# Optimization experiments

Measured on AMD Instinct MI355X. Metric: run time of the kernel, lower is better.

The kernel has to match this reference:

```python
import jax, jax.numpy as jnp
import numpy as np

S_LEN = 256   # seq_len
B = 512       # batch
STATE = 32    # state_dim
ZD = 64       # z_dim
RNN = 512     # rnn_dim
HD = 512      # h_dim
LOG2PI = float(np.log(2.0 * np.pi))


def setup_inputs() -> dict:
    key = jax.random.key(0)
    ks = jax.random.split(key, 12)

    def mat(k, shape, fan_in):
        return jax.random.normal(k, shape, dtype=jnp.float32) * (1.0 / np.sqrt(fan_in))

    z32 = lambda *s: jnp.zeros(s, jnp.float32)
    return {
        "states": jax.random.normal(ks[0], (S_LEN, B, STATE), jnp.float32),
        "z": jax.random.normal(ks[1], (B, ZD), jnp.float32),
        # GRU layer 0: input = concat(state, action) -> 2*STATE
        "Wih0": mat(ks[2], (3 * RNN, 2 * STATE), 2 * STATE),
        "Whh0": mat(ks[3], (3 * RNN, RNN), RNN),
        "bih0": z32(3 * RNN),
        "bhh0": z32(3 * RNN),
        # GRU layer 1: input = hidden of layer 0
        "Wih1": mat(ks[4], (3 * RNN, RNN), RNN),
        "Whh1": mat(ks[5], (3 * RNN, RNN), RNN),
        "bih1": z32(3 * RNN),
        "bhh1": z32(3 * RNN),
        # dec_action_fc: Linear(STATE+ZD+RNN -> HD), ReLU, Linear(HD -> HD), ReLU
        "Wfc1": mat(ks[6], (HD, STATE + ZD + RNN), STATE + ZD + RNN),
        "bfc1": z32(HD),
        "Wfc2": mat(ks[7], (HD, HD), HD),
        "bfc2": z32(HD),
        "Wmean": mat(ks[8], (STATE, HD), HD),
        "bmean": z32(STATE),
        "Wlv": mat(ks[9], (STATE, HD), HD),
        "blv": z32(STATE),
    }


def _gru_step(x, h, Wih, Whh, bih, bhh):
    # PyTorch GRUCell math
    gi = x @ Wih.T + bih  # [B, 3R]
    gh = h @ Whh.T + bhh
    ir, iz, inn = jnp.split(gi, 3, axis=1)
    hr, hz, hn = jnp.split(gh, 3, axis=1)
    r = jax.nn.sigmoid(ir + hr)
    zg = jax.nn.sigmoid(iz + hz)
    n = jnp.tanh(inn + r * hn)
    return (1.0 - zg) * n + zg * h


def reference(states, z, Wih0, Whh0, bih0, bhh0, Wih1, Whh1, bih1, bhh1,
              Wfc1, bfc1, Wfc2, bfc2, Wmean, bmean, Wlv, blv):
    # actions[t] = states[t+1] - states[t]
    actions = states[1:] - states[:-1]
    # loop runs for actions.size(0)-1 = T-2 steps using (states[t], actions[t])
    xs = (states[:-2], actions[:-1])
    Bb = z.shape[0]
    R = Whh0.shape[1]
    h_init = jnp.zeros((2, Bb, R), states.dtype)
    nll_init = jnp.zeros((Bb, states.shape[-1]), states.dtype)

    def step(carry, xt):
        h, nll = carry
        s, a = xt  # [B, STATE] each
        # decode_action: cat(state, z, hidden[-1]) -> MLP -> mean, logvar
        fc_in = jnp.concatenate([s, z, h[1]], axis=1)
        dh = jax.nn.relu(fc_in @ Wfc1.T + bfc1)
        dh = jax.nn.relu(dh @ Wfc2.T + bfc2)
        mean = dh @ Wmean.T + bmean
        logvar = dh @ Wlv.T + blv
        # nll -= Normal(mean, logvar).log_prob(action), std = exp(0.5*logvar)
        nll_t = 0.5 * ((a - mean) ** 2 * jnp.exp(-logvar) + logvar + LOG2PI)
        # update_hidden_state with cat(state, action) through 2-layer GRU
        x_in = jnp.concatenate([s, a], axis=1)
        h0n = _gru_step(x_in, h[0], Wih0, Whh0, bih0, bhh0)
        h1n = _gru_step(h0n, h[1], Wih1, Whh1, bih1, bhh1)
        return (jnp.stack([h0n, h1n]), nll + nll_t), None

    (h, nll), _ = jax.lax.scan(step, (h_init, nll_init), xs)
    return nll  # accumulated NLL, shape [B, STATE]
```

## Files before the change

### kernel.cpp

```cpp
#include <hip/hip_runtime.h>
#include <math.h>

#define BATCH 512
#define LOG2PI 1.8378770664093453f
#define HB 262144

typedef __attribute__((ext_vector_type(8))) short bfrag;
typedef __attribute__((ext_vector_type(4))) float f32x4;
typedef __attribute__((ext_vector_type(4))) unsigned int u32x4;

#define MFMA(a,b,c) __builtin_amdgcn_mfma_f32_16x16x32_bf16(a,b,c,0,0,0)
#define ASTORE(p,v) __hip_atomic_store((p),(v),__ATOMIC_RELAXED,__HIP_MEMORY_SCOPE_AGENT)
#define ALOAD(p)    __hip_atomic_load((p),__ATOMIC_RELAXED,__HIP_MEMORY_SCOPE_AGENT)

__device__ __forceinline__ void st16_sc1(void* p, u32x4 v){
  asm volatile("global_store_dwordx4 %0, %1, off sc1" :: "v"(p), "v"(v) : "memory");
}

__device__ __forceinline__ float sigm(float x){ return 1.0f/(1.0f+__expf(-x)); }
__device__ __forceinline__ unsigned short f2bf(float f){
  unsigned int u = __builtin_bit_cast(unsigned int, f);
  u += 0x7FFFu + ((u>>16)&1u);
  return (unsigned short)(u>>16);
}
__device__ __forceinline__ bfrag cvt8(const float* __restrict__ p){
  bfrag v;
  #pragma unroll
  for (int e=0;e<8;++e) v[e] = (short)f2bf(p[e]);
  return v;
}
__device__ __forceinline__ bfrag cvt8d(const float* __restrict__ p1, const float* __restrict__ p0){
  bfrag v;
  #pragma unroll
  for (int e=0;e<8;++e) v[e] = (short)f2bf(p1[e]-p0[e]);
  return v;
}

struct Params {
  const float *states, *zin;
  const float *Wih0, *Whh0, *bih0, *bhh0;
  const float *Wih1, *Whh1, *bih1, *bhh1;
  const float *Wfc1, *bfc1, *Wfc2, *bfc2;
  const float *Wmean, *bmean, *Wlv, *blv;
  unsigned short *act;
  float *out;
};

__global__ __launch_bounds__(256, 1) void fused(Params P, unsigned* flags) {
  __shared__ unsigned short sm[74752];
  const int tid  = threadIdx.x;
  const int lane = tid & 63;
  const int wv   = tid >> 6;
  const int r16  = lane & 15, kg = lane >> 4;
  const int blk  = blockIdx.x;
  const int xg   = blk & 7, sub = blk >> 3;

  unsigned short* h0 = P.act;
  unsigned short* h1 = P.act +  8*(size_t)HB;
  unsigned short* d1 = P.act + 16*(size_t)HB;
  unsigned short* d2 = P.act + 24*(size_t)HB;

  if (xg < 4) {
    const int jt = sub;
    const float* Wsrc[2] = {P.Wih1, P.Whh1};
    #pragma unroll
    for (int m = 0; m < 2; ++m) {
      const float* W = Wsrc[m];
      for (int c = tid; c < 3072; c += 256) {
        int g = c >> 10, rem = c & 1023;
        int r = rem >> 6, k = (rem & 63) << 3;
        *(bfrag*)&sm[(g*16+r)*1032 + m*512 + k] =
          cvt8(&W[((size_t)(g*512 + jt*16 + r))*512 + k]);
      }
    }
  } else if (xg < 6) {
    const int jt = sub;
    for (int c = tid; c < 384; c += 256) {
      int g = c >> 7, rem = c & 127;
      int r = rem >> 3, k = (rem & 7) << 3;
      *(bfrag*)&sm[(g*16+r)*584 + k] =
        cvt8(&P.Wih0[((size_t)(g*512 + jt*16 + r))*64 + k]);
    }
    for (int c = tid; c < 3072; c += 256) {
      int g = c >> 10, rem = c & 1023;
      int r = rem >> 6, k = (rem & 63) << 3;
      *(bfrag*)&sm[(g*16+r)*584 + 64 + k] =
        cvt8(&P.Whh0[((size_t)(g*512 + jt*16 + r))*512 + k]);
    }
  } else if (xg == 6) {
    const int bn = (sub & 7) * 64;
    const int bmB = (sub >> 3) * 128;
    for (int c = tid; c < 4864; c += 256) {
      int n = c / 76, k = (c % 76) << 3;
      *(bfrag*)&sm[n*616 + k] = cvt8(&P.Wfc1[(size_t)(bn + n)*608 + k]);
    }
    for (int c = tid; c < 1024; c += 256) {
      int r = c >> 3, k = (c & 7) << 3;
      *(bfrag*)&sm[47616 + r*64 + k] = cvt8(&P.zin[(size_t)(bmB + r)*64 + k]);
    }
  } else {
    const int bn = (sub & 7) * 64;
    for (int c = tid; c < 4096; c += 256) {
      int n = c >> 6, k = (c & 63) << 3;
      *(bfrag*)&sm[n*520 + k] = cvt8(&P.Wfc2[(size_t)(bn + n)*512 + k]);
    }
    for (int c = tid; c < 4096; c += 256) {
      int m = c >> 6, k = (c & 63) << 3;
      const float* src = (m < 32) ? &P.Wmean[(size_t)m*512 + k]
                                  : &P.Wlv[(size_t)(m-32)*512 + k];
      *(bfrag*)&sm[33280 + m*520 + k] = cvt8(src);
    }
  }

  float b0 = 0.f, b1 = 0.f, b2 = 0.f, b3 = 0.f;
  if (xg < 4) {
    int j = sub*16 + r16;
    b0 = P.bih1[j] + P.bhh1[j];
    b1 = P.bih1[j+512] + P.bhh1[j+512];
    b2 = P.bih1[j+1024]; b3 = P.bhh1[j+1024];
  } else if (xg < 6) {
    int j = sub*16 + r16;
    b0 = P.bih0[j] + P.bhh0[j];
    b1 = P.bih0[j+512] + P.bhh0[j+512];
    b2 = P.bih0[j+1024]; b3 = P.bhh0[j+1024];
  } else if (xg == 6) {
    int nn0 = (sub & 7)*64 + (wv&1)*32 + r16;
    b0 = P.bfc1[nn0]; b1 = P.bfc1[nn0+16];
  } else {
    int nn0 = (sub & 7)*64 + (wv&1)*32 + r16;
    b0 = P.bfc2[nn0]; b1 = P.bfc2[nn0+16];
    int c = wv*16 + r16;
    b2 = (c < 32) ? P.bmean[c] : P.blv[c-32];
  }
  float hs[4][4] = {};
  float nacc0 = 0.f, nacc1 = 0.f;

  for (int u = 0; u <= 256; ++u) {
    if (wv == 0) {
      int pb1 = -1, pb2 = -1;
      const unsigned t1 = (unsigned)u, t2 = (unsigned)(u - 6);
      if (xg >= 4 && xg < 6) {
        if (u >= 1 && lane < 32) pb1 = lane*8 + xg;
        if (u >= 7)              pb2 = (lane>>1)*8 + 2*(xg-4) + (lane&1);
      } else if (xg < 4) {
        if (u >= 1) pb1 = (lane < 32) ? lane*8 + xg : (lane-32)*8 + 4 + (xg>>1);
        if (u >= 7 && lane < 8) pb2 = (xg*8 + lane)*8 + 6;
      } else if (xg == 6) {
        if (u >= 1 && lane < 32) pb1 = lane*8 + (sub>>3);
        if (u >= 7 && lane < 8)  pb2 = ((sub & ~7) + lane)*8 + 7;
      } else {
        if (u >= 1 && lane < 16) pb1 = ((sub & ~7) + (lane&7))*8 + ((lane<8)?6:7);
      }
      unsigned spin = 0;
      while (true) {
        bool ok = true;
        if (pb1 >= 0) ok &= (ALOAD(&flags[pb1*16]) >= t1);
        if (pb2 >= 0) ok &= (ALOAD(&flags[pb2*16]) >= t2);
        if (__all(ok)) break;
        if (++spin > (1u<<26)) break;
        __builtin_amdgcn_s_sleep(1);
      }
    }
    __syncthreads();
    if (tid < 64) __builtin_amdgcn_fence(__ATOMIC_ACQUIRE, "agent");
    __syncthreads();

    const int ju  = u & 7;
    const int jm1 = (u+7) & 7;
    const int jm2 = (u+6) & 7;
    const int jm3 = (u+5) & 7;

    if (xg < 4) {
      if (u >= 1 && u <= 254) {
        const int jt = sub, bmB = xg * 128;
        const unsigned short* h0r = h0 + (size_t)jm1*HB;
        const unsigned short* h1r = h1 + (size_t)jm2*HB;
        f32x4 R[2]={}, Z[2]={}, NI[2]={}, NH[2]={};
        const int row0 = bmB + wv*32 + r16;
        #pragma unroll
        for (int half = 0; half < 2; ++half) {
          const unsigned short* asrc = half ? h1r : h0r;
          #pragma unroll 4
          for (int kt = 0; kt < 16; ++kt) {
            const int kk = kt*32 + kg*8;
            const int kl = half*512 + kk;
            bfrag a0 = *(const bfrag*)&asrc[(size_t)row0*512 + kk];
            bfrag a1 = *(const bfrag*)&asrc[(size_t)(row0+16)*512 + kk];
            bfrag bR = *(const bfrag*)&sm[(0*16+r16)*1032 + kl];
            bfrag bZ = *(const bfrag*)&sm[(1*16+r16)*1032 + kl];
            bfrag bN = *(const bfrag*)&sm[(2*16+r16)*1032 + kl];
            R[0]=MFMA(a0,bR,R[0]); R[1]=MFMA(a1,bR,R[1]);
            Z[0]=MFMA(a0,bZ,Z[0]); Z[1]=MFMA(a1,bZ,Z[1]);
            if (!half) { NI[0]=MFMA(a0,bN,NI[0]); NI[1]=MFMA(a1,bN,NI[1]); }
            else       { NH[0]=MFMA(a0,bN,NH[0]); NH[1]=MFMA(a1,bN,NH[1]); }
          }
        }
        unsigned short* exch = sm + 49536;
        #pragma unroll
        for (int fm = 0; fm < 2; ++fm)
          #pragma unroll
          for (int e = 0; e < 4; ++e) {
            int rl = wv*32 + fm*16 + kg*4 + e;
            float r  = sigm(R[fm][e] + b0);
            float zg = sigm(Z[fm][e] + b1);
            float nn = tanhf(NI[fm][e] + b2 + r*(NH[fm][e] + b3));
            float hn = (1.f - zg)*nn + zg*hs[fm][e];
            hs[fm][e] = hn;
            exch[rl*16 + r16] = f2bf(hn);
          }
        __syncthreads();
        {
          unsigned short* dst = h1 + (size_t)jm1*HB;
          int r = tid >> 1, hc = tid & 1;
          u32x4 v = *(const u32x4*)&exch[r*16 + hc*8];
          st16_sc1(dst + ((size_t)(bmB + r))*512 + jt*16 + hc*8, v);
        }
      }
    } else if (xg < 6) {
      if (u <= 253) {
        const int jt = sub, bmB = (xg - 4) * 256;
        const unsigned short* h0r = h0 + (size_t)jm1*HB;
        const float* s0p = P.states + (size_t)u*BATCH*32;
        f32x4 R[4]={}, Z[4]={}, NI[4]={}, NH[4]={};
        #pragma unroll
        for (int ks = 0; ks < 2; ++ks) {
          const int kl = ks*32 + kg*8;
          bfrag a[4];
          #pragma unroll
          for (int fm = 0; fm < 4; ++fm) {
            int row = bmB + wv*64 + fm*16 + r16;
            a[fm] = (ks == 0)
              ? cvt8(&s0p[(size_t)row*32 + kg*8])
              : cvt8d(&s0p[(size_t)(BATCH + row)*32 + kg*8], &s0p[(size_t)row*32 + kg*8]);
          }
          bfrag bR = *(const bfrag*)&sm[(0*16+r16)*584 + kl];
          bfrag bZ = *(const bfrag*)&sm[(1*16+r16)*584 + kl];
          bfrag bN = *(const bfrag*)&sm[(2*16+r16)*584 + kl];
          #pragma unroll
          for (int fm = 0; fm < 4; ++fm) {
            R[fm]=MFMA(a[fm],bR,R[fm]); Z[fm]=MFMA(a[fm],bZ,Z[fm]); NI[fm]=MFMA(a[fm],bN,NI[fm]);
          }
        }
        #pragma unroll 2
        for (int kt = 0; kt < 16; ++kt) {
          const int kk = kt*32 + kg*8;
          const int kl = 64 + kk;
          bfrag a[4];
          #pragma unroll
          for (int fm = 0; fm < 4; ++fm) {
            int row = bmB + wv*64 + fm*16 + r16;
            a[fm] = *(const bfrag*)&h0r[(size_t)row*512 + kk];
          }
          bfrag bR = *(const bfrag*)&sm[(0*16+r16)*584 + kl];
          bfrag bZ = *(const bfrag*)&sm[(1*16+r16)*584 + kl];
          bfrag bN = *(const bfrag*)&sm[(2*16+r16)*584 + kl];
          #pragma unroll
          for (int fm = 0; fm < 4; ++fm) {
            R[fm]=MFMA(a[fm],bR,R[fm]); Z[fm]=MFMA(a[fm],bZ,Z[fm]); NH[fm]=MFMA(a[fm],bN,NH[fm]);
          }
        }
        unsigned short* exch = sm + 28032;
        #pragma unroll
        for (int fm = 0; fm < 4; ++fm)
          #pragma unroll
          for (int e = 0; e < 4; ++e) {
            int rl = wv*64 + fm*16 + kg*4 + e;
            float r  = sigm(R[fm][e] + b0);
            float zg = sigm(Z[fm][e] + b1);
            float nn = tanhf(NI[fm][e] + b2 + r*(NH[fm][e] + b3));
            float hn = (1.f - zg)*nn + zg*hs[fm][e];
            hs[fm][e] = hn;
            exch[rl*16 + r16] = f2bf(hn);
          }
        __syncthreads();
        {
          unsigned short* dst = h0 + (size_t)ju*HB;
          int r = tid;
          u32x4 v0 = *(const u32x4*)&exch[r*16];
          u32x4 v1 = *(const u32x4*)&exch[r*16 + 8];
          unsigned short* dp = dst + ((size_t)(bmB + r))*512 + jt*16;
          st16_sc1(dp,     v0);
          st16_sc1(dp + 8, v1);
        }
      }
    } else if (xg == 6) {
      if (u >= 1 && u <= 254) {
        const int bmB = (sub >> 3) * 128, bnB = (sub & 7) * 64;
        const unsigned short* h1r = h1 + (size_t)jm2*HB;
        const float* s0p = P.states + (size_t)(u-1)*BATCH*32;
        f32x4 acc[4][2] = {};
        const int arow = bmB + (wv>>1)*64;
        const int bcol = (wv&1)*32;
        #pragma unroll 2
        for (int kt = 0; kt < 19; ++kt) {
          const int k = kt*32 + kg*8;
          bfrag a[4];
          #pragma unroll
          for (int fm = 0; fm < 4; ++fm) {
            int row = arow + fm*16 + r16;
            int rl  = row - bmB;
            if (kt == 0)      a[fm] = cvt8(&s0p[(size_t)row*32 + k]);
            else if (kt <= 2) a[fm] = *(const bfrag*)&sm[47616 + rl*64 + (k - 32)];
            else              a[fm] = *(const bfrag*)&h1r[(size_t)row*512 + (k - 96)];
          }
          bfrag bf0 = *(const bfrag*)&sm[(bcol      + r16)*616 + k];
          bfrag bf1 = *(const bfrag*)&sm[(bcol + 16 + r16)*616 + k];
          #pragma unroll
          for (int fm = 0; fm < 4; ++fm) {
            acc[fm][0] = MFMA(a[fm], bf0, acc[fm][0]);
            acc[fm][1] = MFMA(a[fm], bf1, acc[fm][1]);
          }
        }
        unsigned short* exch = sm + 39424;
        #pragma unroll
        for (int fm = 0; fm < 4; ++fm)
          #pragma unroll
          for (int fn = 0; fn < 2; ++fn) {
            float bias = fn ? b1 : b0;
            #pragma unroll
            for (int e = 0; e < 4; ++e) {
              int rl = (wv>>1)*64 + fm*16 + kg*4 + e;
              int cl = bcol + fn*16 + r16;
              exch[rl*64 + cl] = f2bf(fmaxf(acc[fm][fn][e] + bias, 0.f));
            }
          }
        __syncthreads();
        {
          unsigned short* dst = d1 + (size_t)jm1*HB;
          int r = tid >> 1, hc = tid & 1;
          #pragma unroll
          for (int q = 0; q < 4; ++q) {
            u32x4 v = *(const u32x4*)&exch[r*64 + hc*32 + q*8];
            st16_sc1(dst + ((size_t)(bmB + r))*512 + bnB + hc*32 + q*8, v);
          }
        }
        __syncthreads();
      }
    } else {
      if (u >= 2 && u <= 255) {
        const int bmB = (sub >> 3) * 128, bnB = (sub & 7) * 64;
        const unsigned short* dr = d1 + (size_t)jm2*HB;
        f32x4 acc[4][2] = {};
        const int arow = bmB + (wv>>1)*64;
        const int bcol = (wv&1)*32;
        #pragma unroll 2
        for (int kt = 0; kt < 16; ++kt) {
          const int k = kt*32 + kg*8;
          bfrag a[4];
          #pragma unroll
          for (int fm = 0; fm < 4; ++fm) {
            int row = arow + fm*16 + r16;
            a[fm] = *(const bfrag*)&dr[(size_t)row*512 + k];
          }
          bfrag bf0 = *(const bfrag*)&sm[(bcol      + r16)*520 + k];
          bfrag bf1 = *(const bfrag*)&sm[(bcol + 16 + r16)*520 + k];
          #pragma unroll
          for (int fm = 0; fm < 4; ++fm) {
            acc[fm][0] = MFMA(a[fm], bf0, acc[fm][0]);
            acc[fm][1] = MFMA(a[fm], bf1, acc[fm][1]);
          }
        }
        unsigned short* exch = sm + 66560;
        #pragma unroll
        for (int fm = 0; fm < 4; ++fm)
          #pragma unroll
          for (int fn = 0; fn < 2; ++fn) {
            float bias = fn ? b1 : b0;
            #pragma unroll
            for (int e = 0; e < 4; ++e) {
              int rl = (wv>>1)*64 + fm*16 + kg*4 + e;
              int cl = bcol + fn*16 + r16;
              exch[rl*64 + cl] = f2bf(fmaxf(acc[fm][fn][e] + bias, 0.f));
            }
          }
        __syncthreads();
        {
          unsigned short* dst = d2 + (size_t)jm2*HB;
          int r = tid >> 1, hc = tid & 1;
          #pragma unroll
          for (int q = 0; q < 4; ++q) {
            u32x4 v = *(const u32x4*)&exch[r*64 + hc*32 + q*8];
            st16_sc1(dst + ((size_t)(bmB + r))*512 + bnB + hc*32 + q*8, v);
          }
        }
      }
      if (u >= 3) {
        const int t = u - 3;
        const unsigned short* dr = d2 + (size_t)jm3*HB;
        f32x4 acc = {};
        #pragma unroll 2
        for (int kt = 0; kt < 16; ++kt) {
          const int k = kt*32 + kg*8;
          bfrag a = *(const bfrag*)&dr[(size_t)(sub*16 + r16)*512 + k];
          bfrag b = *(const bfrag*)&sm[33280 + (wv*16 + r16)*520 + k];
          acc = MFMA(a, b, acc);
        }
        __syncthreads();
        float* exch = (float*)(sm + 66560);
        const int c = wv*16 + r16;
        #pragma unroll
        for (int e = 0; e < 4; ++e)
          exch[(kg*4+e)*66 + c] = acc[e] + b2;
        __syncthreads();
        const float* s0p = P.states + (size_t)t*BATCH*32;
        #pragma unroll
        for (int e2 = 0; e2 < 2; ++e2) {
          int idx = tid*2 + e2;
          int r = idx >> 5, i = idx & 31;
          int b = sub*16 + r;
          float mean = exch[r*66 + i], lv = exch[r*66 + 32 + i];
          float av = s0p[(size_t)(BATCH + b)*32 + i] - s0p[(size_t)b*32 + i];
          float d = av - mean;
          float v = 0.5f*(d*d*__expf(-lv) + lv + LOG2PI);
          if (e2) nacc1 += v; else nacc0 += v;
        }
      }
    }

    __syncthreads();
    if (tid == 0) ASTORE(&flags[blk*16], (unsigned)(u+1));
  }

  if (xg == 7) {
    #pragma unroll
    for (int e2 = 0; e2 < 2; ++e2) {
      int idx = tid*2 + e2;
      int b = sub*16 + (idx >> 5), i = idx & 31;
      P.out[(size_t)b*32 + i] = e2 ? nacc1 : nacc0;
    }
  }
}

extern "C" void kernel_launch(void* const* d_in, const int* in_sizes, int n_in,
                              void* d_out, int out_size, void* d_ws, size_t ws_size,
                              hipStream_t stream) {
  Params P;
  P.states = (const float*)d_in[0];
  P.zin    = (const float*)d_in[1];
  P.Wih0   = (const float*)d_in[2];
  P.Whh0   = (const float*)d_in[3];
  P.bih0   = (const float*)d_in[4];
  P.bhh0   = (const float*)d_in[5];
  P.Wih1   = (const float*)d_in[6];
  P.Whh1   = (const float*)d_in[7];
  P.bih1   = (const float*)d_in[8];
  P.bhh1   = (const float*)d_in[9];
  P.Wfc1   = (const float*)d_in[10];
  P.bfc1   = (const float*)d_in[11];
  P.Wfc2   = (const float*)d_in[12];
  P.bfc2   = (const float*)d_in[13];
  P.Wmean  = (const float*)d_in[14];
  P.bmean  = (const float*)d_in[15];
  P.Wlv    = (const float*)d_in[16];
  P.blv    = (const float*)d_in[17];
  P.out = (float*)d_out;
  P.act = (unsigned short*)d_ws;

  unsigned* flags = (unsigned*)(P.act + 32*(size_t)HB);

  hipMemsetAsync(P.act, 0, 16*(size_t)HB*sizeof(unsigned short), stream);
  hipMemsetAsync(flags, 0, 256*16*sizeof(unsigned), stream);
  hipMemsetAsync(d_out, 0, (size_t)out_size*sizeof(float), stream);

  fused<<<dim3(256), dim3(256), 0, stream>>>(P, flags);
}
```

Before: 4.339 ms.

## Use per-XCD leader block polling with local broadcast flag for step sync

Only block sub==0 in each xg group now polls the full set of cross-block producer flags. It then publishes a per-group step counter, and the other blocks in that group spin on that single flag and invalidate their cache before proceeding. The aim is to cut global atomic polling traffic from many blocks hammering the same flags. In exchange it adds a serial hop, leader then followers, to every step's sync latency. It also widens the leader's wait sets so that each leader covers every producer its group needs.

```diff
diff --git a/kernel.cpp b/kernel.cpp
--- a/kernel.cpp
+++ b/kernel.cpp
@@ -46,7 +46,7 @@
   float *out;
 };
 
-__global__ __launch_bounds__(256, 1) void fused(Params P, unsigned* flags) {
+__global__ __launch_bounds__(256, 1) void fused(Params P, unsigned* flags, unsigned* xcdf) {
   __shared__ unsigned short sm[74752];
   const int tid  = threadIdx.x;
   const int lane = tid & 63;
@@ -136,34 +136,50 @@
   float nacc0 = 0.f, nacc1 = 0.f;
 
   for (int u = 0; u <= 256; ++u) {
-    if (wv == 0) {
-      int pb1 = -1, pb2 = -1;
-      const unsigned t1 = (unsigned)u, t2 = (unsigned)(u - 6);
-      if (xg >= 4 && xg < 6) {
-        if (u >= 1 && lane < 32) pb1 = lane*8 + xg;
-        if (u >= 7)              pb2 = (lane>>1)*8 + 2*(xg-4) + (lane&1);
-      } else if (xg < 4) {
-        if (u >= 1) pb1 = (lane < 32) ? lane*8 + xg : (lane-32)*8 + 4 + (xg>>1);
-        if (u >= 7 && lane < 8) pb2 = (xg*8 + lane)*8 + 6;
-      } else if (xg == 6) {
-        if (u >= 1 && lane < 32) pb1 = lane*8 + (sub>>3);
-        if (u >= 7 && lane < 8)  pb2 = ((sub & ~7) + lane)*8 + 7;
-      } else {
-        if (u >= 1 && lane < 16) pb1 = ((sub & ~7) + (lane&7))*8 + ((lane<8)?6:7);
-      }
-      unsigned spin = 0;
-      while (true) {
-        bool ok = true;
-        if (pb1 >= 0) ok &= (ALOAD(&flags[pb1*16]) >= t1);
-        if (pb2 >= 0) ok &= (ALOAD(&flags[pb2*16]) >= t2);
-        if (__all(ok)) break;
-        if (++spin > (1u<<26)) break;
-        __builtin_amdgcn_s_sleep(1);
-      }
-    }
-    __syncthreads();
-    if (tid < 64) __builtin_amdgcn_fence(__ATOMIC_ACQUIRE, "agent");
-    __syncthreads();
+    if (sub == 0) {
+      if (wv == 0) {
+        int pb1 = -1, pb2 = -1, pb3 = -1;
+        const unsigned t1 = (unsigned)u, t2 = (unsigned)(u - 6);
+        if (xg >= 4 && xg < 6) {
+          if (u >= 1 && lane < 32) pb1 = lane*8 + xg;
+          if (u >= 7)              pb2 = (lane>>1)*8 + 2*(xg-4) + (lane&1);
+        } else if (xg < 4) {
+          if (u >= 1) pb1 = (lane < 32) ? lane*8 + xg : (lane-32)*8 + 4 + (xg>>1);
+          if (u >= 7 && lane < 8) pb2 = (xg*8 + lane)*8 + 6;
+        } else if (xg == 6) {
+          if (u >= 1) { pb1 = (lane>>2)*8 + (lane&3); pb3 = pb1 + 128; }
+          if (u >= 7 && lane < 32) pb2 = lane*8 + 7;
+        } else {
+          if (u >= 1) pb1 = (lane < 32) ? lane*8 + 6 : (lane-32)*8 + 7;
+        }
+        unsigned spin = 0;
+        while (true) {
+          bool ok = true;
+          if (pb1 >= 0) ok &= (ALOAD(&flags[pb1*16]) >= t1);
+          if (pb3 >= 0) ok &= (ALOAD(&flags[pb3*16]) >= t1);
+          if (pb2 >= 0) ok &= (ALOAD(&flags[pb2*16]) >= t2);
+          if (__all(ok)) break;
+          if (++spin > (1u<<26)) break;
+          __builtin_amdgcn_s_sleep(1);
+        }
+      }
+      __syncthreads();
+      if (tid < 64) __builtin_amdgcn_fence(__ATOMIC_ACQUIRE, "agent");
+      __syncthreads();
+      if (tid == 0) ASTORE(&xcdf[xg*16], (unsigned)(u+1));
+    } else {
+      if (wv == 0 && lane == 0) {
+        unsigned spin = 0;
+        while (ALOAD(&xcdf[xg*16]) < (unsigned)(u+1)) {
+          if (++spin > (1u<<26)) break;
+          __builtin_amdgcn_s_sleep(1);
+        }
+      }
+      __syncthreads();
+      if (tid < 64)
+        asm volatile("buffer_inv\n\ts_waitcnt vmcnt(0)" ::: "memory");
+      __syncthreads();
+    }
 
     const int ju  = u & 7;
     const int jm1 = (u+7) & 7;
@@ -457,10 +473,11 @@
   P.act = (unsigned short*)d_ws;
 
   unsigned* flags = (unsigned*)(P.act + 32*(size_t)HB);
+  unsigned* xcdf  = flags + 256*16;
 
   hipMemsetAsync(P.act, 0, 16*(size_t)HB*sizeof(unsigned short), stream);
-  hipMemsetAsync(flags, 0, 256*16*sizeof(unsigned), stream);
+  hipMemsetAsync(flags, 0, (256*16 + 8*16)*sizeof(unsigned), stream);
   hipMemsetAsync(d_out, 0, (size_t)out_size*sizeof(float), stream);
 
-  fused<<<dim3(256), dim3(256), 0, stream>>>(P, flags);
-}
+  fused<<<dim3(256), dim3(256), 0, stream>>>(P, flags, xcdf);
+}
```

New measurement: 3.994 ms (median of 2 runs). -7.9%, faster.

## Shrink activation ring buffers, add local copies, tighten cross-block flag dependencies

Applied to the files above, without the earlier changes.

Cuts the global activation rings from 8 slots to 4 and adds 2-slot local copies of h0, h1 and d2 for consumers that only need data written by the same block group. Cross-block readers use volatile loads, and the acquire fence becomes a buffer_inv plus waitcnt. Wait conditions are rewritten with three flag slots and a shorter lag (u-2 instead of u-6), and the spin timeout drops. The aim is cheaper synchronization and smaller cache footprint. The risk is that the tighter slot reuse and the lighter invalidate could race, producing stale or overwritten data.

```diff
diff --git a/kernel.cpp b/kernel.cpp
--- a/kernel.cpp
+++ b/kernel.cpp
@@ -15,6 +15,10 @@
 
 __device__ __forceinline__ void st16_sc1(void* p, u32x4 v){
   asm volatile("global_store_dwordx4 %0, %1, off sc1" :: "v"(p), "v"(v) : "memory");
+}
+__device__ __forceinline__ bfrag vlb(const unsigned short* p){
+  u32x4 v = *(const volatile u32x4*)p;
+  union { u32x4 u; bfrag b; } c; c.u = v; return c.b;
 }
 
 __device__ __forceinline__ float sigm(float x){ return 1.0f/(1.0f+__expf(-x)); }
@@ -55,10 +59,12 @@
   const int blk  = blockIdx.x;
   const int xg   = blk & 7, sub = blk >> 3;
 
-  unsigned short* h0 = P.act;
-  unsigned short* h1 = P.act +  8*(size_t)HB;
-  unsigned short* d1 = P.act + 16*(size_t)HB;
-  unsigned short* d2 = P.act + 24*(size_t)HB;
+  unsigned short* h0G = P.act;
+  unsigned short* h1G = P.act +  4*(size_t)HB;
+  unsigned short* d1G = P.act +  8*(size_t)HB;
+  unsigned short* h0L = P.act + 12*(size_t)HB;
+  unsigned short* h1L = P.act + 14*(size_t)HB;
+  unsigned short* d2L = P.act + 16*(size_t)HB;
 
   if (xg < 4) {
     const int jt = sub;
@@ -137,63 +143,76 @@
 
   for (int u = 0; u <= 256; ++u) {
     if (wv == 0) {
-      int pb1 = -1, pb2 = -1;
-      const unsigned t1 = (unsigned)u, t2 = (unsigned)(u - 6);
+      int pA=-1, pB=-1, pC=-1; unsigned tA=0, tB=0, tC=0;
       if (xg >= 4 && xg < 6) {
-        if (u >= 1 && lane < 32) pb1 = lane*8 + xg;
-        if (u >= 7)              pb2 = (lane>>1)*8 + 2*(xg-4) + (lane&1);
+        if (u >= 1 && lane < 32) { pA = lane*8 + xg; tA = u; }
+        if (u >= 4) {
+          int s = lane & 31, x0 = (lane >> 5) * 2;
+          pB = s*8 + x0;     tB = u-2;
+          pC = s*8 + x0 + 1; tC = u-2;
+        }
       } else if (xg < 4) {
-        if (u >= 1) pb1 = (lane < 32) ? lane*8 + xg : (lane-32)*8 + 4 + (xg>>1);
-        if (u >= 7 && lane < 8) pb2 = (xg*8 + lane)*8 + 6;
+        if (u >= 1) {
+          if (lane < 32) { pA = lane*8 + xg; tA = u; }
+          else           { pB = (lane-32)*8 + 4 + (xg>>1); tB = u; }
+        }
+        if (u >= 5 && lane < 8) { pC = (xg*8 + lane)*8 + 6; tC = u-2; }
       } else if (xg == 6) {
-        if (u >= 1 && lane < 32) pb1 = lane*8 + (sub>>3);
-        if (u >= 7 && lane < 8)  pb2 = ((sub & ~7) + lane)*8 + 7;
+        if (u >= 1 && lane < 32) { pA = lane*8 + (sub>>3); tA = u; }
+        if (u >= 5 && lane >= 32) { pB = (lane-32)*8 + 7; tB = u-2; }
       } else {
-        if (u >= 1 && lane < 16) pb1 = ((sub & ~7) + (lane&7))*8 + ((lane<8)?6:7);
+        if (u >= 2) {
+          if (lane < 8)   { pA = ((sub & ~7) + lane)*8 + 6; tA = u; }
+          if (lane >= 32 && lane < 40)
+                          { pB = ((sub & ~7) + (lane-32))*8 + 7; tB = u; }
+        }
       }
       unsigned spin = 0;
       while (true) {
         bool ok = true;
-        if (pb1 >= 0) ok &= (ALOAD(&flags[pb1*16]) >= t1);
-        if (pb2 >= 0) ok &= (ALOAD(&flags[pb2*16]) >= t2);
+        if (pA >= 0) ok &= (ALOAD(&flags[pA*16]) >= tA);
+        if (pB >= 0) ok &= (ALOAD(&flags[pB*16]) >= tB);
+        if (pC >= 0) ok &= (ALOAD(&flags[pC*16]) >= tC);
         if (__all(ok)) break;
-        if (++spin > (1u<<26)) break;
+        if (++spin > (1u<<20)) break;
         __builtin_amdgcn_s_sleep(1);
       }
     }
     __syncthreads();
-    if (tid < 64) __builtin_amdgcn_fence(__ATOMIC_ACQUIRE, "agent");
+    if (tid < 64) asm volatile("buffer_inv\n\ts_waitcnt vmcnt(0)" ::: "memory");
     __syncthreads();
-
-    const int ju  = u & 7;
-    const int jm1 = (u+7) & 7;
-    const int jm2 = (u+6) & 7;
-    const int jm3 = (u+5) & 7;
 
     if (xg < 4) {
       if (u >= 1 && u <= 254) {
         const int jt = sub, bmB = xg * 128;
-        const unsigned short* h0r = h0 + (size_t)jm1*HB;
-        const unsigned short* h1r = h1 + (size_t)jm2*HB;
+        const unsigned short* h0r = h0G + (size_t)((u+3)&3)*HB;
+        const unsigned short* h1r = h1L + (size_t)(u&1)*HB;
         f32x4 R[2]={}, Z[2]={}, NI[2]={}, NH[2]={};
         const int row0 = bmB + wv*32 + r16;
-        #pragma unroll
-        for (int half = 0; half < 2; ++half) {
-          const unsigned short* asrc = half ? h1r : h0r;
-          #pragma unroll 4
-          for (int kt = 0; kt < 16; ++kt) {
-            const int kk = kt*32 + kg*8;
-            const int kl = half*512 + kk;
-            bfrag a0 = *(const bfrag*)&asrc[(size_t)row0*512 + kk];
-            bfrag a1 = *(const bfrag*)&asrc[(size_t)(row0+16)*512 + kk];
-            bfrag bR = *(const bfrag*)&sm[(0*16+r16)*1032 + kl];
-            bfrag bZ = *(const bfrag*)&sm[(1*16+r16)*1032 + kl];
-            bfrag bN = *(const bfrag*)&sm[(2*16+r16)*1032 + kl];
-            R[0]=MFMA(a0,bR,R[0]); R[1]=MFMA(a1,bR,R[1]);
-            Z[0]=MFMA(a0,bZ,Z[0]); Z[1]=MFMA(a1,bZ,Z[1]);
-            if (!half) { NI[0]=MFMA(a0,bN,NI[0]); NI[1]=MFMA(a1,bN,NI[1]); }
-            else       { NH[0]=MFMA(a0,bN,NH[0]); NH[1]=MFMA(a1,bN,NH[1]); }
-          }
+        #pragma unroll 4
+        for (int kt = 0; kt < 16; ++kt) {
+          const int kk = kt*32 + kg*8;
+          bfrag a0 = vlb(h0r + (size_t)row0*512 + kk);
+          bfrag a1 = vlb(h0r + (size_t)(row0+16)*512 + kk);
+          bfrag bR = *(const bfrag*)&sm[(0*16+r16)*1032 + kk];
+          bfrag bZ = *(const bfrag*)&sm[(1*16+r16)*1032 + kk];
+          bfrag bN = *(const bfrag*)&sm[(2*16+r16)*1032 + kk];
+          R[0]=MFMA(a0,bR,R[0]); R[1]=MFMA(a1,bR,R[1]);
+          Z[0]=MFMA(a0,bZ,Z[0]); Z[1]=MFMA(a1,bZ,Z[1]);
+          NI[0]=MFMA(a0,bN,NI[0]); NI[1]=MFMA(a1,bN,NI[1]);
+        }
+        #pragma unroll 4
+        for (int kt = 0; kt < 16; ++kt) {
+          const int kk = kt*32 + kg*8;
+          const int kl = 512 + kk;
+          bfrag a0 = *(const bfrag*)&h1r[(size_t)row0*512 + kk];
+          bfrag a1 = *(const bfrag*)&h1r[(size_t)(row0+16)*512 + kk];
+          bfrag bR = *(const bfrag*)&sm[(0*16+r16)*1032 + kl];
+          bfrag bZ = *(const bfrag*)&sm[(1*16+r16)*1032 + kl];
+          bfrag bN = *(const bfrag*)&sm[(2*16+r16)*1032 + kl];
+          R[0]=MFMA(a0,bR,R[0]); R[1]=MFMA(a1,bR,R[1]);
+          Z[0]=MFMA(a0,bZ,Z[0]); Z[1]=MFMA(a1,bZ,Z[1]);
+          NH[0]=MFMA(a0,bN,NH[0]); NH[1]=MFMA(a1,bN,NH[1]);
         }
         unsigned short* exch = sm + 49536;
         #pragma unroll
@@ -210,16 +229,17 @@
           }
         __syncthreads();
         {
-          unsigned short* dst = h1 + (size_t)jm1*HB;
           int r = tid >> 1, hc = tid & 1;
           u32x4 v = *(const u32x4*)&exch[r*16 + hc*8];
-          st16_sc1(dst + ((size_t)(bmB + r))*512 + jt*16 + hc*8, v);
+          size_t off = ((size_t)(bmB + r))*512 + jt*16 + hc*8;
+          *(u32x4*)&h1L[(size_t)((u+1)&1)*HB + off] = v;
+          st16_sc1(h1G + (size_t)((u+3)&3)*HB + off, v);
         }
       }
     } else if (xg < 6) {
       if (u <= 253) {
         const int jt = sub, bmB = (xg - 4) * 256;
-        const unsigned short* h0r = h0 + (size_t)jm1*HB;
+        const unsigned short* h0r = h0L + (size_t)((u+1)&1)*HB;
         const float* s0p = P.states + (size_t)u*BATCH*32;
         f32x4 R[4]={}, Z[4]={}, NI[4]={}, NH[4]={};
         #pragma unroll
@@ -274,19 +294,20 @@
           }
         __syncthreads();
         {
-          unsigned short* dst = h0 + (size_t)ju*HB;
           int r = tid;
           u32x4 v0 = *(const u32x4*)&exch[r*16];
           u32x4 v1 = *(const u32x4*)&exch[r*16 + 8];
-          unsigned short* dp = dst + ((size_t)(bmB + r))*512 + jt*16;
-          st16_sc1(dp,     v0);
-          st16_sc1(dp + 8, v1);
+          size_t off = ((size_t)(bmB + r))*512 + jt*16;
+          *(u32x4*)&h0L[(size_t)(u&1)*HB + off]     = v0;
+          *(u32x4*)&h0L[(size_t)(u&1)*HB + off + 8] = v1;
+          st16_sc1(h0G + (size_t)(u&3)*HB + off,     v0);
+          st16_sc1(h0G + (size_t)(u&3)*HB + off + 8, v1);
         }
       }
     } else if (xg == 6) {
       if (u >= 1 && u <= 254) {
         const int bmB = (sub >> 3) * 128, bnB = (sub & 7) * 64;
-        const unsigned short* h1r = h1 + (size_t)jm2*HB;
+        const unsigned short* h1r = h1G + (size_t)((u+2)&3)*HB;
         const float* s0p = P.states + (size_t)(u-1)*BATCH*32;
         f32x4 acc[4][2] = {};
         const int arow = bmB + (wv>>1)*64;
@@ -301,7 +322,7 @@
             int rl  = row - bmB;
             if (kt == 0)      a[fm] = cvt8(&s0p[(size_t)row*32 + k]);
             else if (kt <= 2) a[fm] = *(const bfrag*)&sm[47616 + rl*64 + (k - 32)];
-            else              a[fm] = *(const bfrag*)&h1r[(size_t)row*512 + (k - 96)];
+            else              a[fm] = vlb(h1r + (size_t)row*512 + (k - 96));
           }
           bfrag bf0 = *(const bfrag*)&sm[(bcol      + r16)*616 + k];
           bfrag bf1 = *(const bfrag*)&sm[(bcol + 16 + r16)*616 + k];
@@ -326,12 +347,11 @@
           }
         __syncthreads();
         {
-          unsigned short* dst = d1 + (size_t)jm1*HB;
           int r = tid >> 1, hc = tid & 1;
           #pragma unroll
           for (int q = 0; q < 4; ++q) {
             u32x4 v = *(const u32x4*)&exch[r*64 + hc*32 + q*8];
-            st16_sc1(dst + ((size_t)(bmB + r))*512 + bnB + hc*32 + q*8, v);
+            st16_sc1(d1G + (size_t)((u+3)&3)*HB + ((size_t)(bmB + r))*512 + bnB + hc*32 + q*8, v);
           }
         }
         __syncthreads();
@@ -339,7 +359,7 @@
     } else {
       if (u >= 2 && u <= 255) {
         const int bmB = (sub >> 3) * 128, bnB = (sub & 7) * 64;
-        const unsigned short* dr = d1 + (size_t)jm2*HB;
+        const unsigned short* dr = d1G + (size_t)((u+2)&3)*HB;
         f32x4 acc[4][2] = {};
         const int arow = bmB + (wv>>1)*64;
         const int bcol = (wv&1)*32;
@@ -348,10 +368,8 @@
           const int k = kt*32 + kg*8;
           bfrag a[4];
           #pragma unroll
-          for (int fm = 0; fm < 4; ++fm) {
-            int row = arow + fm*16 + r16;
-            a[fm] = *(const bfrag*)&dr[(size_t)row*512 + k];
-          }
+          for (int fm = 0; fm < 4; ++fm)
+            a[fm] = vlb(dr + (size_t)(arow + fm*16 + r16)*512 + k);
           bfrag bf0 = *(const bfrag*)&sm[(bcol      + r16)*520 + k];
           bfrag bf1 = *(const bfrag*)&sm[(bcol + 16 + r16)*520 + k];
           #pragma unroll
@@ -375,18 +393,17 @@
           }
         __syncthreads();
         {
-          unsigned short* dst = d2 + (size_t)jm2*HB;
           int r = tid >> 1, hc = tid & 1;
           #pragma unroll
           for (int q = 0; q < 4; ++q) {
             u32x4 v = *(const u32x4*)&exch[r*64 + hc*32 + q*8];
-            st16_sc1(dst + ((size_t)(bmB + r))*512 + bnB + hc*32 + q*8, v);
+            *(u32x4*)&d2L[(size_t)(u&1)*HB + ((size_t)(bmB + r))*512 + bnB + hc*32 + q*8] = v;
           }
         }
       }
       if (u >= 3) {
         const int t = u - 3;
-        const unsigned short* dr = d2 + (size_t)jm3*HB;
+        const unsigned short* dr = d2L + (size_t)((u+1)&1)*HB;
         f32x4 acc = {};
         #pragma unroll 2
         for (int kt = 0; kt < 16; ++kt) {
@@ -456,9 +473,10 @@
   P.out = (float*)d_out;
   P.act = (unsigned short*)d_ws;
 
-  unsigned* flags = (unsigned*)(P.act + 32*(size_t)HB);
-
-  hipMemsetAsync(P.act, 0, 16*(size_t)HB*sizeof(unsigned short), stream);
+  unsigned* flags = (unsigned*)(P.act + 18*(size_t)HB);
+
+  hipMemsetAsync(P.act, 0, 8*(size_t)HB*sizeof(unsigned short), stream);
+  hipMemsetAsync(P.act + 12*(size_t)HB, 0, 4*(size_t)HB*sizeof(unsigned short), stream);
   hipMemsetAsync(flags, 0, 256*16*sizeof(unsigned), stream);
   hipMemsetAsync(d_out, 0, (size_t)out_size*sizeof(float), stream);
 
```

Result: slower. 4.691 ms (+8.1%).
